# Optimization experiments

Measured on AMD Instinct MI355X. Metric: run time of the kernel, lower is better.

Reference implementation:

```python
import jax, jax.numpy as jnp
import numpy as np

B, T, D, H, K, DEPTH = 2, 2048, 512, 8, 16, 3
EPS = 1e-5


def setup_inputs() -> dict:
    key = jax.random.key(0)
    ks = jax.random.split(key, 6)
    s = 0.02
    return {
        "x": jax.random.normal(ks[0], (B, T, D), jnp.float32),
        "ln1_s": jnp.ones((DEPTH, D), jnp.float32),
        "ln1_b": jnp.zeros((DEPTH, D), jnp.float32),
        "qkv_w": jax.random.normal(ks[1], (DEPTH, D, 3 * D), jnp.float32) * s,
        "proj_w": jax.random.normal(ks[2], (DEPTH, D, D), jnp.float32) * s,
        "proj_b": jnp.zeros((DEPTH, D), jnp.float32),
        "ln2_s": jnp.ones((DEPTH, D), jnp.float32),
        "ln2_b": jnp.zeros((DEPTH, D), jnp.float32),
        "w1": jax.random.normal(ks[3], (DEPTH, D, 4 * D), jnp.float32) * s,
        "b1": jnp.zeros((DEPTH, 4 * D), jnp.float32),
        "w2": jax.random.normal(ks[4], (DEPTH, 4 * D, D), jnp.float32) * s,
        "b2": jnp.zeros((DEPTH, D), jnp.float32),
    }


def _ln(x, s, b):
    m = x.mean(-1, keepdims=True)
    v = ((x - m) ** 2).mean(-1, keepdims=True)
    return (x - m) * jax.lax.rsqrt(v + EPS) * s + b


def _dilated_mask(t, dil):
    # allowed key j for query i: j = i - step*dil, step in [0, K), j >= 0
    i = jnp.arange(t)[:, None]
    j = jnp.arange(t)[None, :]
    diff = i - j
    ok = (diff >= 0) & (diff % dil == 0) & (diff < K * dil)
    return jnp.where(ok, 0.0, -jnp.inf).astype(jnp.float32)


def reference(x, ln1_s, ln1_b, qkv_w, proj_w, proj_b, ln2_s, ln2_b, w1, b1, w2, b2):
    hd = D // H
    scale = hd ** -0.5
    for d in range(DEPTH):
        dil = 2 ** d
        h = _ln(x, ln1_s[d], ln1_b[d])
        qkv = (h @ qkv_w[d]).reshape(B, T, 3, H, hd).transpose(2, 0, 3, 1, 4)
        q, k, v = qkv[0], qkv[1], qkv[2]  # each (B,H,T,hd)
        attn = jnp.einsum('bhid,bhjd->bhij', q, k) * scale + _dilated_mask(T, dil)
        o = jnp.einsum('bhij,bhjd->bhid', jax.nn.softmax(attn, axis=-1), v)
        o = o.transpose(0, 2, 1, 3).reshape(B, T, D) @ proj_w[d] + proj_b[d]
        x = x + o
        h = _ln(x, ln2_s[d], ln2_b[d])
        x = x + (jax.nn.gelu(h @ w1[d] + b1[d], approximate=False) @ w2[d] + b2[d])
    return x
```

## Files before the change

### kernel.cpp

```cpp
#include <hip/hip_runtime.h>
#include <math.h>

#define TSEQ   2048
#define DM     512
#define NH     8
#define HD     64
#define KATT   16
#define NDEPTH 3
#define MROWS  4096

typedef __attribute__((ext_vector_type(8))) short bf16x8;
typedef __attribute__((ext_vector_type(8))) unsigned short u16x8;
typedef __attribute__((ext_vector_type(4))) float f32x4;

static __device__ __forceinline__ unsigned short f2b(float f) {
    unsigned int u = __float_as_uint(f);
    unsigned int r = (u + 0x7fffu + ((u >> 16) & 1u)) >> 16;
    return (unsigned short)r;
}
static __device__ __forceinline__ float b2f(unsigned short s) {
    return __uint_as_float((unsigned int)s << 16);
}

static __device__ __forceinline__ void load_lds16(const void* g, void* l) {
    __builtin_amdgcn_global_load_lds(
        (const __attribute__((address_space(1))) unsigned int*)g,
        (__attribute__((address_space(3))) unsigned int*)l, 16, 0, 0);
}

__global__ __launch_bounds__(256) void transpose_all_kernel(
    const float* __restrict__ qkv_w, const float* __restrict__ proj_w,
    const float* __restrict__ w1,    const float* __restrict__ w2,
    unsigned short* __restrict__ qkvT, unsigned short* __restrict__ projT,
    unsigned short* __restrict__ w1T,  unsigned short* __restrict__ w2T)
{
    int id = blockIdx.x;
    const float* W; unsigned short* Wt; int Kd, Nd;
    if (id < 2304)      { W = qkv_w;  Wt = qkvT;  Kd = 512;  Nd = 1536; }
    else if (id < 3072) { W = proj_w; Wt = projT; Kd = 512;  Nd = 512;  id -= 2304; }
    else if (id < 6144) { W = w1;     Wt = w1T;   Kd = 512;  Nd = 2048; id -= 3072; }
    else                { W = w2;     Wt = w2T;   Kd = 2048; Nd = 512;  id -= 6144; }
    const int nt = Nd >> 5, per = nt * (Kd >> 5);
    const int d = id / per, rem = id % per;
    const int k0 = (rem / nt) * 32, n0 = (rem % nt) * 32;

    __shared__ float tile[32][33];
    const size_t off = (size_t)d * Kd * Nd;
    const float* Wd = W + off;
    unsigned short* Wtd = Wt + off;
    const int tx = threadIdx.x, ty = threadIdx.y;
#pragma unroll
    for (int r = 0; r < 32; r += 8)
        tile[ty + r][tx] = Wd[(size_t)(k0 + ty + r) * Nd + (n0 + tx)];
    __syncthreads();
#pragma unroll
    for (int r = 0; r < 32; r += 8)
        Wtd[(size_t)(n0 + ty + r) * Kd + (k0 + tx)] = f2b(tile[tx][ty + r]);
}

__global__ __launch_bounds__(256) void ln_kernel(
    const float* __restrict__ x, const float* __restrict__ sc,
    const float* __restrict__ bi, unsigned short* __restrict__ h)
{
    const int wid  = blockIdx.x * 4 + (threadIdx.x >> 6);
    const int lane = threadIdx.x & 63;
    const float* xr = x + (size_t)wid * DM;
    const float4 v0 = *(const float4*)&xr[lane * 4];
    const float4 v1 = *(const float4*)&xr[256 + lane * 4];
    float s = v0.x + v0.y + v0.z + v0.w + v1.x + v1.y + v1.z + v1.w;
    float q = v0.x*v0.x + v0.y*v0.y + v0.z*v0.z + v0.w*v0.w
            + v1.x*v1.x + v1.y*v1.y + v1.z*v1.z + v1.w*v1.w;
#pragma unroll
    for (int off = 32; off; off >>= 1) {
        s += __shfl_xor(s, off, 64);
        q += __shfl_xor(q, off, 64);
    }
    const float mean = s * (1.0f / DM);
    const float var  = q * (1.0f / DM) - mean * mean;
    const float rs   = rsqrtf(var + 1e-5f);
    unsigned short* hr = h + (size_t)wid * DM;
    const int c0 = lane * 4, c1 = 256 + lane * 4;
    ushort4 o0, o1;
    o0.x = f2b((v0.x - mean) * rs * sc[c0+0] + bi[c0+0]);
    o0.y = f2b((v0.y - mean) * rs * sc[c0+1] + bi[c0+1]);
    o0.z = f2b((v0.z - mean) * rs * sc[c0+2] + bi[c0+2]);
    o0.w = f2b((v0.w - mean) * rs * sc[c0+3] + bi[c0+3]);
    o1.x = f2b((v1.x - mean) * rs * sc[c1+0] + bi[c1+0]);
    o1.y = f2b((v1.y - mean) * rs * sc[c1+1] + bi[c1+1]);
    o1.z = f2b((v1.z - mean) * rs * sc[c1+2] + bi[c1+2]);
    o1.w = f2b((v1.w - mean) * rs * sc[c1+3] + bi[c1+3]);
    *(ushort4*)&hr[c0] = o0;
    *(ushort4*)&hr[c1] = o1;
}

__global__ __launch_bounds__(256) void attn_kernel(
    const unsigned short* __restrict__ qh, const unsigned short* __restrict__ kh,
    const unsigned short* __restrict__ vh, unsigned short* __restrict__ o, int dil)
{
    const int blk  = blockIdx.x;
    const int tile = blk & (TSEQ / 16 - 1);
    const int bh   = blk >> 7;
    const int b    = bh >> 3, hh = bh & 7;
    const int t0   = tile * 16;
    const int wave = threadIdx.x >> 6, lane = threadIdx.x & 63;
    const int tq   = wave * 4 + (lane >> 4);
    const int s    = lane & 15;
    const int t    = t0 + tq;
    const size_t slab = ((size_t)hh * MROWS + (size_t)b * TSEQ) * HD;

    __shared__ float p_lds[16][17];

    int row = t - s * dil;
    const bool valid = (row >= 0);
    row = max(row, 0);
    const u16x8* kr = (const u16x8*)(kh + slab + (size_t)row * HD);
    const u16x8* qr = (const u16x8*)(qh + slab + (size_t)t * HD);
    float dot = 0.0f;
#pragma unroll
    for (int j = 0; j < 8; j++) {
        const u16x8 kk = kr[j];
        const u16x8 qq = qr[j];
#pragma unroll
        for (int e = 0; e < 8; e++) dot += b2f(qq[e]) * b2f(kk[e]);
    }
    const float sc = valid ? dot * 0.125f : -1e30f;
    float m = sc;
#pragma unroll
    for (int off = 1; off < 16; off <<= 1) m = fmaxf(m, __shfl_xor(m, off, 64));
    const float p = expf(sc - m);
    float l = p;
#pragma unroll
    for (int off = 1; off < 16; off <<= 1) l += __shfl_xor(l, off, 64);
    p_lds[tq][s] = p / l;
    __syncthreads();

#pragma unroll
    for (int qi = 0; qi < 4; qi++) {
        const int qq = qi * 4 + wave;
        const int tt = t0 + qq;
        float acc = 0.0f;
#pragma unroll
        for (int ss = 0; ss < KATT; ss++) {
            int vr = tt - ss * dil;
            const float pw = p_lds[qq][ss];
            vr = max(vr, 0);
            acc += pw * b2f(vh[slab + (size_t)vr * HD + lane]);
        }
        o[(size_t)(b * TSEQ + tt) * DM + (size_t)hh * HD + lane] = f2b(acc);
    }
}

template<int EPI, int TN>
__global__ __launch_bounds__(256) void gemm_kernel(
    const unsigned short* __restrict__ A,
    const unsigned short* __restrict__ Bt,
    const float* __restrict__ bias,
    unsigned short* __restrict__ outp,
    unsigned short* __restrict__ outb,
    unsigned short* __restrict__ outq,
    unsigned short* __restrict__ outk,
    unsigned short* __restrict__ outv,
    int N, int K, int Kslice, size_t zstride)
{
    constexpr int FN = TN / 32;
    constexpr int CA = 2;
    constexpr int CB = TN / 64;
    const int tid  = threadIdx.x;
    const int wave = tid >> 6, lane = tid & 63;
    const int bm = blockIdx.y * 128;
    const int bn = blockIdx.x * TN;
    const int wm = (wave >> 1) * 64;
    const int wn = (wave & 1) * (TN / 2);
    const int ml = lane & 15, quad = lane >> 4;
    const int kbeg = blockIdx.z * Kslice;

    __shared__ unsigned short As[2][128 * 32];
    __shared__ unsigned short Bs[2][TN * 32];

    f32x4 acc[4][FN] = {};

    const int rr = lane >> 2, ss = lane & 3;
    const int cc = ((ss - (rr >> 1)) & 3) * 8;
    const unsigned short* Aa[CA];
    const unsigned short* Bb[CB];
#pragma unroll
    for (int j = 0; j < CA; j++)
        Aa[j] = A + (size_t)(bm + (wave * CA + j) * 16 + rr) * K + kbeg + cc;
#pragma unroll
    for (int j = 0; j < CB; j++)
        Bb[j] = Bt + (size_t)(bn + (wave * CB + j) * 16 + rr) * K + kbeg + cc;

    const int fslot = ((quad + (ml >> 1)) & 3) * 8;

#pragma unroll
    for (int j = 0; j < CA; j++)
        load_lds16(Aa[j], &As[0][(wave * CA + j) * 512]);
#pragma unroll
    for (int j = 0; j < CB; j++)
        load_lds16(Bb[j], &Bs[0][(wave * CB + j) * 512]);
    __syncthreads();

    const int steps = Kslice >> 5;
    for (int s = 0; s < steps; s++) {
        const int cur = s & 1, nxt = cur ^ 1;
        const bool more = (s + 1 < steps);
        if (more) {
            const int k0 = (s + 1) * 32;
#pragma unroll
            for (int j = 0; j < CA; j++)
                load_lds16(Aa[j] + k0, &As[nxt][(wave * CA + j) * 512]);
#pragma unroll
            for (int j = 0; j < CB; j++)
                load_lds16(Bb[j] + k0, &Bs[nxt][(wave * CB + j) * 512]);
        }

        bf16x8 af[4], bfr[FN];
#pragma unroll
        for (int i = 0; i < 4; i++)
            af[i] = *(const bf16x8*)&As[cur][(wm + i * 16 + ml) * 32 + fslot];
#pragma unroll
        for (int j = 0; j < FN; j++)
            bfr[j] = *(const bf16x8*)&Bs[cur][(wn + j * 16 + ml) * 32 + fslot];

#pragma unroll
        for (int i = 0; i < 4; i++)
#pragma unroll
            for (int j = 0; j < FN; j++)
                acc[i][j] = __builtin_amdgcn_mfma_f32_16x16x32_bf16(
                    af[i], bfr[j], acc[i][j], 0, 0, 0);

        if (more) __syncthreads();
    }

    unsigned short* op = outp + (size_t)blockIdx.z * zstride;
#pragma unroll
    for (int i = 0; i < 4; i++)
#pragma unroll
        for (int j = 0; j < FN; j++)
#pragma unroll
            for (int r = 0; r < 4; r++) {
                const int row = bm + wm + i * 16 + quad * 4 + r;
                const int col = bn + wn + j * 16 + ml;
                const float v = acc[i][j][r];
                if (EPI == 0) {
                    op[(size_t)row * N + col] = f2b(v);
                } else if (EPI == 2) {
                    const float u = v + bias[col];
                    const float g = 0.5f * u * (1.0f + erff(u * 0.70710678118654752f));
                    outb[(size_t)row * N + col] = f2b(g);
                } else {
                    const int which = col >> 9;
                    const int hh = (col & 511) >> 6;
                    const int dim = col & 63;
                    unsigned short* dst =
                        which == 0 ? outq : (which == 1 ? outk : outv);
                    dst[((size_t)hh * MROWS + row) * HD + dim] = f2b(v);
                }
            }
}

template<bool DO_LN, int Z>
__global__ __launch_bounds__(256) void reduce_kernel(
    const float* __restrict__ xin,
    const unsigned short* __restrict__ part,
    const float* __restrict__ bias,
    const float* __restrict__ lns, const float* __restrict__ lnb,
    float* __restrict__ xout, unsigned short* __restrict__ h)
{
    const int wid  = blockIdx.x * 4 + (threadIdx.x >> 6);
    const int lane = threadIdx.x & 63;
    const int c0 = lane * 4, c1 = 256 + lane * 4;
    const size_t ro = (size_t)wid * DM;

    float4 a0 = *(const float4*)&xin[ro + c0];
    float4 a1 = *(const float4*)&xin[ro + c1];
#pragma unroll
    for (int z = 0; z < Z; z++) {
        const unsigned short* p = part + (size_t)z * (MROWS * (size_t)DM) + ro;
        const ushort4 p0 = *(const ushort4*)&p[c0];
        const ushort4 p1 = *(const ushort4*)&p[c1];
        a0.x += b2f(p0.x); a0.y += b2f(p0.y); a0.z += b2f(p0.z); a0.w += b2f(p0.w);
        a1.x += b2f(p1.x); a1.y += b2f(p1.y); a1.z += b2f(p1.z); a1.w += b2f(p1.w);
    }
    a0.x += bias[c0+0]; a0.y += bias[c0+1]; a0.z += bias[c0+2]; a0.w += bias[c0+3];
    a1.x += bias[c1+0]; a1.y += bias[c1+1]; a1.z += bias[c1+2]; a1.w += bias[c1+3];

    *(float4*)&xout[ro + c0] = a0;
    *(float4*)&xout[ro + c1] = a1;

    if (DO_LN) {
        float s = a0.x + a0.y + a0.z + a0.w + a1.x + a1.y + a1.z + a1.w;
        float q = a0.x*a0.x + a0.y*a0.y + a0.z*a0.z + a0.w*a0.w
                + a1.x*a1.x + a1.y*a1.y + a1.z*a1.z + a1.w*a1.w;
#pragma unroll
        for (int off = 32; off; off >>= 1) {
            s += __shfl_xor(s, off, 64);
            q += __shfl_xor(q, off, 64);
        }
        const float mean = s * (1.0f / DM);
        const float var  = q * (1.0f / DM) - mean * mean;
        const float rs   = rsqrtf(var + 1e-5f);
        unsigned short* hr = h + ro;
        ushort4 o0, o1;
        o0.x = f2b((a0.x - mean) * rs * lns[c0+0] + lnb[c0+0]);
        o0.y = f2b((a0.y - mean) * rs * lns[c0+1] + lnb[c0+1]);
        o0.z = f2b((a0.z - mean) * rs * lns[c0+2] + lnb[c0+2]);
        o0.w = f2b((a0.w - mean) * rs * lns[c0+3] + lnb[c0+3]);
        o1.x = f2b((a1.x - mean) * rs * lns[c1+0] + lnb[c1+0]);
        o1.y = f2b((a1.y - mean) * rs * lns[c1+1] + lnb[c1+1]);
        o1.z = f2b((a1.z - mean) * rs * lns[c1+2] + lnb[c1+2]);
        o1.w = f2b((a1.w - mean) * rs * lns[c1+3] + lnb[c1+3]);
        *(ushort4*)&hr[c0] = o0;
        *(ushort4*)&hr[c1] = o1;
    }
}

extern "C" void kernel_launch(void* const* d_in, const int* in_sizes, int n_in,
                              void* d_out, int out_size, void* d_ws, size_t ws_size,
                              hipStream_t stream)
{
    (void)in_sizes; (void)n_in; (void)out_size; (void)ws_size;
    const float* x_in   = (const float*)d_in[0];
    const float* ln1_s  = (const float*)d_in[1];
    const float* ln1_b  = (const float*)d_in[2];
    const float* qkv_w  = (const float*)d_in[3];
    const float* proj_w = (const float*)d_in[4];
    const float* proj_b = (const float*)d_in[5];
    const float* ln2_s  = (const float*)d_in[6];
    const float* ln2_b  = (const float*)d_in[7];
    const float* w1     = (const float*)d_in[8];
    const float* b1     = (const float*)d_in[9];
    const float* w2     = (const float*)d_in[10];
    const float* b2     = (const float*)d_in[11];

    char* ws = (char*)d_ws;
    float*          xbuf = (float*)(ws);
    unsigned short* qhb  = (unsigned short*)(ws + 8388608);
    unsigned short* khb  = (unsigned short*)(ws + 12582912);
    unsigned short* vhb  = (unsigned short*)(ws + 16777216);
    unsigned short* ubuf = (unsigned short*)(ws + 33554432);
    unsigned short* hbuf = (unsigned short*)(ws + 50331648);
    unsigned short* obuf = (unsigned short*)(ws + 54525952);
    unsigned short* part = (unsigned short*)(ws + 58720256);
    unsigned short* qkvT = (unsigned short*)(ws + 92274688);
    unsigned short* projT= (unsigned short*)(ws + 96993280);
    unsigned short* w1T  = (unsigned short*)(ws + 98566144);
    unsigned short* w2T  = (unsigned short*)(ws + 104857600);

    const size_t ZS = (size_t)MROWS * DM;

    transpose_all_kernel<<<9216, dim3(32, 8), 0, stream>>>(
        qkv_w, proj_w, w1, w2, qkvT, projT, w1T, w2T);

    ln_kernel<<<MROWS / 4, 256, 0, stream>>>(x_in, ln1_s, ln1_b, hbuf);

    for (int d = 0; d < NDEPTH; d++) {
        const int dil = 1 << d;
        const float* xin = (d == 0) ? x_in : xbuf;

        gemm_kernel<3, 64><<<dim3(1536/64, MROWS/128, 1), 256, 0, stream>>>(
            hbuf, qkvT + (size_t)d * 1536 * 512, nullptr, nullptr, nullptr,
            qhb, khb, vhb, 1536, 512, 512, 0);
        attn_kernel<<<2 * NH * (TSEQ / 16), 256, 0, stream>>>(qhb, khb, vhb, obuf, dil);
        gemm_kernel<0, 64><<<dim3(512/64, MROWS/128, 2), 256, 0, stream>>>(
            obuf, projT + (size_t)d * 512 * 512, nullptr, part, nullptr,
            nullptr, nullptr, nullptr, 512, 512, 256, ZS);
        reduce_kernel<true, 2><<<MROWS / 4, 256, 0, stream>>>(
            xin, part, proj_b + d * DM, ln2_s + d * DM, ln2_b + d * DM,
            xbuf, hbuf);
        gemm_kernel<2, 128><<<dim3(2048/128, MROWS/128, 1), 256, 0, stream>>>(
            hbuf, w1T + (size_t)d * 2048 * 512, b1 + d * 2048, nullptr, ubuf,
            nullptr, nullptr, nullptr, 2048, 512, 512, 0);
        gemm_kernel<0, 128><<<dim3(512/128, MROWS/128, 4), 256, 0, stream>>>(
            ubuf, w2T + (size_t)d * 512 * 2048, nullptr, part, nullptr,
            nullptr, nullptr, nullptr, 512, 2048, 512, ZS);
        if (d < NDEPTH - 1) {
            reduce_kernel<true, 4><<<MROWS / 4, 256, 0, stream>>>(
                xbuf, part, b2 + d * DM, ln1_s + (d+1) * DM, ln1_b + (d+1) * DM,
                xbuf, hbuf);
        } else {
            reduce_kernel<false, 4><<<MROWS / 4, 256, 0, stream>>>(
                xbuf, part, b2 + d * DM, nullptr, nullptr,
                (float*)d_out, nullptr);
        }
    }
}
```

Measured before the change: 389.0 us.

## Stage attention K/V/Q in LDS, fuse prep kernels, use fast erf

```diff
diff --git a/kernel.cpp b/kernel.cpp
--- a/kernel.cpp
+++ b/kernel.cpp
@@ -28,42 +28,54 @@
         (__attribute__((address_space(3))) unsigned int*)l, 16, 0, 0);
 }
 
-__global__ __launch_bounds__(256) void transpose_all_kernel(
+static __device__ __forceinline__ float fast_erf(float x) {
+    const float a  = fabsf(x);
+    const float t  = 1.0f / (1.0f + 0.3275911f * a);
+    const float p  = t * (0.254829592f + t * (-0.284496736f +
+                     t * (1.421413741f + t * (-1.453152027f + t * 1.061405429f))));
+    const float e  = __expf(-a * a);
+    const float r  = 1.0f - p * e;
+    return __builtin_copysignf(r, x);
+}
+
+__global__ __launch_bounds__(256) void prep_kernel(
     const float* __restrict__ qkv_w, const float* __restrict__ proj_w,
     const float* __restrict__ w1,    const float* __restrict__ w2,
     unsigned short* __restrict__ qkvT, unsigned short* __restrict__ projT,
-    unsigned short* __restrict__ w1T,  unsigned short* __restrict__ w2T)
-{
-    int id = blockIdx.x;
-    const float* W; unsigned short* Wt; int Kd, Nd;
-    if (id < 2304)      { W = qkv_w;  Wt = qkvT;  Kd = 512;  Nd = 1536; }
-    else if (id < 3072) { W = proj_w; Wt = projT; Kd = 512;  Nd = 512;  id -= 2304; }
-    else if (id < 6144) { W = w1;     Wt = w1T;   Kd = 512;  Nd = 2048; id -= 3072; }
-    else                { W = w2;     Wt = w2T;   Kd = 2048; Nd = 512;  id -= 6144; }
-    const int nt = Nd >> 5, per = nt * (Kd >> 5);
-    const int d = id / per, rem = id % per;
-    const int k0 = (rem / nt) * 32, n0 = (rem % nt) * 32;
-
-    __shared__ float tile[32][33];
-    const size_t off = (size_t)d * Kd * Nd;
-    const float* Wd = W + off;
-    unsigned short* Wtd = Wt + off;
-    const int tx = threadIdx.x, ty = threadIdx.y;
-#pragma unroll
-    for (int r = 0; r < 32; r += 8)
-        tile[ty + r][tx] = Wd[(size_t)(k0 + ty + r) * Nd + (n0 + tx)];
-    __syncthreads();
-#pragma unroll
-    for (int r = 0; r < 32; r += 8)
-        Wtd[(size_t)(n0 + ty + r) * Kd + (k0 + tx)] = f2b(tile[tx][ty + r]);
-}
-
-__global__ __launch_bounds__(256) void ln_kernel(
+    unsigned short* __restrict__ w1T,  unsigned short* __restrict__ w2T,
     const float* __restrict__ x, const float* __restrict__ sc,
     const float* __restrict__ bi, unsigned short* __restrict__ h)
 {
-    const int wid  = blockIdx.x * 4 + (threadIdx.x >> 6);
-    const int lane = threadIdx.x & 63;
+    __shared__ float tile[32][33];
+    int id = blockIdx.x;
+    const int tid = threadIdx.x;
+
+    if (id < 9216) {
+        const float* W; unsigned short* Wt; int Kd, Nd;
+        if (id < 2304)      { W = qkv_w;  Wt = qkvT;  Kd = 512;  Nd = 1536; }
+        else if (id < 3072) { W = proj_w; Wt = projT; Kd = 512;  Nd = 512;  id -= 2304; }
+        else if (id < 6144) { W = w1;     Wt = w1T;   Kd = 512;  Nd = 2048; id -= 3072; }
+        else                { W = w2;     Wt = w2T;   Kd = 2048; Nd = 512;  id -= 6144; }
+        const int nt = Nd >> 5, per = nt * (Kd >> 5);
+        const int d = id / per, rem = id % per;
+        const int k0 = (rem / nt) * 32, n0 = (rem % nt) * 32;
+
+        const size_t off = (size_t)d * Kd * Nd;
+        const float* Wd = W + off;
+        unsigned short* Wtd = Wt + off;
+        const int tx = tid & 31, ty = tid >> 5;
+#pragma unroll
+        for (int r = 0; r < 32; r += 8)
+            tile[ty + r][tx] = Wd[(size_t)(k0 + ty + r) * Nd + (n0 + tx)];
+        __syncthreads();
+#pragma unroll
+        for (int r = 0; r < 32; r += 8)
+            Wtd[(size_t)(n0 + ty + r) * Kd + (k0 + tx)] = f2b(tile[tx][ty + r]);
+        return;
+    }
+
+    const int wid  = (id - 9216) * 4 + (tid >> 6);
+    const int lane = tid & 63;
     const float* xr = x + (size_t)wid * DM;
     const float4 v0 = *(const float4*)&xr[lane * 4];
     const float4 v1 = *(const float4*)&xr[256 + lane * 4];
@@ -102,24 +114,43 @@
     const int bh   = blk >> 7;
     const int b    = bh >> 3, hh = bh & 7;
     const int t0   = tile * 16;
-    const int wave = threadIdx.x >> 6, lane = threadIdx.x & 63;
+    const int tid  = threadIdx.x;
+    const int wave = tid >> 6, lane = tid & 63;
     const int tq   = wave * 4 + (lane >> 4);
     const int s    = lane & 15;
     const int t    = t0 + tq;
     const size_t slab = ((size_t)hh * MROWS + (size_t)b * TSEQ) * HD;
 
+    const int R    = 15 * dil + 16;
+    const int base = t0 - 15 * dil;
+
+    __shared__ unsigned short ks[76 * 64];
+    __shared__ unsigned short vs[76 * 64];
+    __shared__ unsigned short qs[16 * 64];
     __shared__ float p_lds[16][17];
 
-    int row = t - s * dil;
-    const bool valid = (row >= 0);
-    row = max(row, 0);
-    const u16x8* kr = (const u16x8*)(kh + slab + (size_t)row * HD);
-    const u16x8* qr = (const u16x8*)(qh + slab + (size_t)t * HD);
+    for (int c = tid; c < R * 8; c += 256) {
+        const int r = c >> 3, cs = c & 7;
+        const int sr = max(base + r, 0);
+        const int ps = ((cs + r + (r >> 2)) & 7) * 8;
+        const size_t g = slab + (size_t)sr * HD + cs * 8;
+        *(u16x8*)&ks[r * 64 + ps] = *(const u16x8*)(kh + g);
+        *(u16x8*)&vs[r * 64 + ps] = *(const u16x8*)(vh + g);
+    }
+    if (tid < 128) {
+        const int r = tid >> 3, cs = tid & 7;
+        *(u16x8*)&qs[r * 64 + cs * 8] =
+            *(const u16x8*)(qh + slab + (size_t)(t0 + r) * HD + cs * 8);
+    }
+    __syncthreads();
+
+    const bool valid = (t - s * dil) >= 0;
+    const int  kidx  = tq + 15 * dil - s * dil;
     float dot = 0.0f;
 #pragma unroll
     for (int j = 0; j < 8; j++) {
-        const u16x8 kk = kr[j];
-        const u16x8 qq = qr[j];
+        const u16x8 kk = *(const u16x8*)&ks[kidx * 64 + (((j + kidx + (kidx >> 2)) & 7) * 8)];
+        const u16x8 qq = *(const u16x8*)&qs[tq * 64 + j * 8];
 #pragma unroll
         for (int e = 0; e < 8; e++) dot += b2f(qq[e]) * b2f(kk[e]);
     }
@@ -137,16 +168,15 @@
 #pragma unroll
     for (int qi = 0; qi < 4; qi++) {
         const int qq = qi * 4 + wave;
-        const int tt = t0 + qq;
         float acc = 0.0f;
 #pragma unroll
         for (int ss = 0; ss < KATT; ss++) {
-            int vr = tt - ss * dil;
+            const int idx = qq + 15 * dil - ss * dil;
             const float pw = p_lds[qq][ss];
-            vr = max(vr, 0);
-            acc += pw * b2f(vh[slab + (size_t)vr * HD + lane]);
+            const int ps = (((lane >> 3) + idx + (idx >> 2)) & 7);
+            acc += pw * b2f(vs[idx * 64 + ps * 8 + (lane & 7)]);
         }
-        o[(size_t)(b * TSEQ + tt) * DM + (size_t)hh * HD + lane] = f2b(acc);
+        o[(size_t)(b * TSEQ + (t0 + qq)) * DM + (size_t)hh * HD + lane] = f2b(acc);
     }
 }
 
@@ -246,7 +276,7 @@
                     op[(size_t)row * N + col] = f2b(v);
                 } else if (EPI == 2) {
                     const float u = v + bias[col];
-                    const float g = 0.5f * u * (1.0f + erff(u * 0.70710678118654752f));
+                    const float g = 0.5f * u * (1.0f + fast_erf(u * 0.70710678118654752f));
                     outb[(size_t)row * N + col] = f2b(g);
                 } else {
                     const int which = col >> 9;
@@ -349,10 +379,9 @@
 
     const size_t ZS = (size_t)MROWS * DM;
 
-    transpose_all_kernel<<<9216, dim3(32, 8), 0, stream>>>(
-        qkv_w, proj_w, w1, w2, qkvT, projT, w1T, w2T);
-
-    ln_kernel<<<MROWS / 4, 256, 0, stream>>>(x_in, ln1_s, ln1_b, hbuf);
+    prep_kernel<<<10240, 256, 0, stream>>>(
+        qkv_w, proj_w, w1, w2, qkvT, projT, w1T, w2T,
+        x_in, ln1_s, ln1_b, hbuf);
 
     for (int d = 0; d < NDEPTH; d++) {
         const int dil = 1 << d;
```

Measured after the change: 390.1 us. No clear change (+0.3%).
